# Optimization experiments

Measured on AMD Instinct MI355X. Metric: run time of the kernel, lower is better.

The kernel has to match this reference:

```python
import jax, jax.numpy as jnp
import numpy as np

MIN_NORM = 1e-15
BALL_EPS = 1e-5  # proj margin, c = 1
HYPER_BETA = 1.0


def _artanh(x):
    x = jnp.clip(x, -1.0 + 1e-7, 1.0 - 1e-7)
    return jnp.arctanh(x)


def _proj(x):
    # clip points inside the unit Poincare ball
    norm = jnp.maximum(jnp.linalg.norm(x, axis=-1, keepdims=True), MIN_NORM)
    maxnorm = 1.0 - BALL_EPS
    return jnp.where(norm > maxnorm, x / norm * maxnorm, x)


def _expmap0(u):
    un = jnp.maximum(jnp.linalg.norm(u, axis=-1, keepdims=True), MIN_NORM)
    return jnp.tanh(un) * u / un


def _mobius_add(x, y):
    x2 = jnp.sum(x * x, axis=-1, keepdims=True)
    y2 = jnp.sum(y * y, axis=-1, keepdims=True)
    xy = jnp.sum(x * y, axis=-1, keepdims=True)
    num = (1.0 + 2.0 * xy + y2) * x + (1.0 - x2) * y
    den = 1.0 + 2.0 * xy + x2 * y2
    return num / jnp.maximum(den, MIN_NORM)


def _sqdist(p, q):
    ma = _mobius_add(-p, q)
    d = 2.0 * _artanh(jnp.linalg.norm(ma, axis=-1))
    return d * d


def _to_klein(x):
    return 2.0 * x / (1.0 + jnp.sum(x * x, axis=-1, keepdims=True))


def _lorentz_factor(x):
    return 1.0 / jnp.sqrt(jnp.maximum(1.0 - jnp.sum(x * x, axis=-1), 1e-7))


def _klein_to(x):
    return x / (1.0 + jnp.sqrt(jnp.maximum(1.0 - jnp.sum(x * x, axis=-1, keepdims=True), 0.0)))


def _logmap0(p):
    pn = jnp.maximum(jnp.linalg.norm(p, axis=-1, keepdims=True), MIN_NORM)
    return _artanh(pn) * p / pn


def setup_inputs() -> dict:
    key = jax.random.key(0)
    k1, k2, k3, k4, k5 = jax.random.split(key, 5)
    B, L, V, D, A, S = 4096, 50, 50000, 200, 14, 30
    inputs = jax.random.randint(k1, (B, L), 0, V, dtype=jnp.int32)
    emb = jax.random.normal(k2, (V, D), dtype=jnp.float32) * 0.1  # w2v * 0.1 as in student_init
    xav = float(np.sqrt(6.0 / (D + D)))
    M = jax.random.uniform(k3, (D, D), dtype=jnp.float32, minval=-xav, maxval=xav)
    a_emb = jax.random.normal(k4, (A, S, D), dtype=jnp.float32) * 0.1
    sw = jax.random.uniform(k5, (A, S), dtype=jnp.float32)
    seed_w = sw / jnp.sum(jnp.abs(sw), axis=1, keepdims=True)  # L1-normalized
    return {"inputs": inputs, "emb": emb, "M": M, "a_emb": a_emb, "seed_w": seed_w}


def reference(inputs, emb, M, a_emb, seed_w):
    # --- AttentionEncoder ---
    x_wrd = emb[inputs]                                   # [B,L,D] gather
    x_avg = jnp.mean(x_wrd, axis=1)                       # [B,D]
    scores = jnp.einsum('bld,de,be->bl', x_wrd, M, x_avg)  # [B,L]
    a = jax.nn.softmax(scores, axis=1)
    enc = jnp.einsum('bl,bld->bd', a, x_wrd)              # [B,D]

    # --- hyperbolic projection ---
    enc = _proj(_expmap0(enc))                            # [B,D] on Poincare ball
    a_emb_w = jnp.sum(a_emb * seed_w[:, :, None], axis=1)  # [A,D]
    hyp_a = _proj(_expmap0(a_emb_w))                      # [A,D]

    sqd = _sqdist(enc[:, None, :], hyp_a[None, :, :])     # [B,A]
    probs_exp = jnp.exp(-HYPER_BETA * sqd - 0.05)         # [B,A]
    a_probs = probs_exp / jnp.sum(probs_exp, axis=1, keepdims=True)

    kle = _to_klein(hyp_a)                                # [A,D]
    lf = _lorentz_factor(kle)                             # [A]
    probs = lf[None, :] * probs_exp                       # [B,A]
    probs_expanded = (probs / jnp.sum(probs, axis=1, keepdims=True))[:, :, None]  # [B,A,1]

    kle_o = jnp.sum(kle[None, :, :] * probs_expanded, axis=1)  # [B,D] Klein barycenter
    r = _klein_to(kle_o)                                  # [B,D]
    eu_r = _logmap0(r)                                    # [B,D]
    return eu_r, probs_expanded, a_probs
```

## Files before the change

### kernel.cpp

```cpp
#include <hip/hip_runtime.h>
#include <hip/hip_fp16.h>
#include <math.h>

#define B_ 4096
#define L_ 50
#define D_ 200
#define A_ 14
#define S_ 30

#define WS_HYP   0
#define WS_KLE   (A_ * D_)
#define WS_Y2    (2 * A_ * D_)
#define WS_LF    (WS_Y2 + A_)
#define WS_MH    8192
#define WS_V     8192

__device__ __forceinline__ float wave_reduce_sum(float v) {
    #pragma unroll
    for (int off = 32; off > 0; off >>= 1) v += __shfl_down(v, off, 64);
    return v;
}
__device__ __forceinline__ float bfly_sum(float v) {
    #pragma unroll
    for (int m = 32; m > 0; m >>= 1) v += __shfl_xor(v, m, 64);
    return v;
}
__device__ __forceinline__ float bfly_max(float v) {
    #pragma unroll
    for (int m = 32; m > 0; m >>= 1) v = fmaxf(v, __shfl_xor(v, m, 64));
    return v;
}
__device__ __forceinline__ float bfly_sum16(float v) {
    #pragma unroll
    for (int m = 8; m > 0; m >>= 1) v += __shfl_xor(v, m, 64);
    return v;
}
__device__ __forceinline__ float block_reduce_512(float val, volatile float* red) {
    __syncthreads();
    val = wave_reduce_sum(val);
    if ((threadIdx.x & 63) == 0) red[threadIdx.x >> 6] = val;
    __syncthreads();
    float s = 0.f;
    #pragma unroll
    for (int i = 0; i < 8; ++i) s += red[i];
    return s;
}

typedef _Float16 h2v __attribute__((ext_vector_type(2)));
__device__ __forceinline__ float fd2(unsigned a, unsigned b, float c) {
#if __has_builtin(__builtin_amdgcn_fdot2)
    return __builtin_amdgcn_fdot2(__builtin_bit_cast(h2v, a),
                                  __builtin_bit_cast(h2v, b), c, false);
#else
    __half2 ha = __builtin_bit_cast(__half2, a), hb = __builtin_bit_cast(__half2, b);
    float2 fa = __half22float2(ha), fb = __half22float2(hb);
    return fmaf(fa.x, fb.x, fmaf(fa.y, fb.y, c));
#endif
}
__device__ __forceinline__ unsigned packh2(float a, float b) {
    __half2 h = __floats2half2_rn(a, b);
    return __builtin_bit_cast(unsigned, h);
}

__global__ __launch_bounds__(256) void precompute_anchors(
    const float* __restrict__ a_emb, const float* __restrict__ seed_w,
    float* __restrict__ ws)
{
    __shared__ float u[A_][D_];
    __shared__ float nrm2[A_];
    const int t = threadIdx.x;
    const int wave = t >> 6, lane = t & 63;

    for (int d = t; d < D_; d += 256) {
        for (int a = 0; a < A_; ++a) {
            float acc = 0.f;
            #pragma unroll 5
            for (int s = 0; s < S_; ++s)
                acc += a_emb[(a * S_ + s) * D_ + d] * seed_w[a * S_ + s];
            u[a][d] = acc;
        }
    }
    __syncthreads();

    for (int a = wave; a < A_; a += 4) {
        float s = 0.f;
        for (int d = lane; d < D_; d += 64) s += u[a][d] * u[a][d];
        s = wave_reduce_sum(s);
        if (lane == 0) nrm2[a] = s;
    }
    __syncthreads();

    float* hyp = ws + WS_HYP;
    float* kle = ws + WS_KLE;
    float* y2  = ws + WS_Y2;
    float* lf  = ws + WS_LF;
    const float maxn = 1.0f - 1e-5f;

    for (int a = 0; a < A_; ++a) {
        float un = fmaxf(sqrtf(nrm2[a]), 1e-15f);
        float th = tanhf(un);
        float pn = fminf(th, maxn);
        float s  = pn / un;
        float py2 = pn * pn;
        float kscale = 2.0f / (1.0f + py2);
        float k2 = py2 * kscale * kscale;
        if (t == 0) {
            y2[a] = py2;
            lf[a] = 1.0f / sqrtf(fmaxf(1.0f - k2, 1e-7f));
        }
        for (int d = t; d < D_; d += 256) {
            float h = u[a][d] * s;
            hyp[a * D_ + d] = h;
            kle[a * D_ + d] = h * kscale;
        }
    }
}

__global__ __launch_bounds__(256) void convert_M(
    const float* __restrict__ M, __half* __restrict__ Mh)
{
    int i = blockIdx.x * 256 + threadIdx.x;
    if (i < D_ * D_) Mh[i] = __float2half(M[i]);
}

__global__ __launch_bounds__(256) void fused_wave(
    const int*   __restrict__ inputs,
    const float* __restrict__ emb,
    const float* __restrict__ ws,
    float* __restrict__ out)
{
    const float*  kle = ws + WS_KLE;
    const float*  y2  = ws + WS_Y2;
    const float*  lf  = ws + WS_LF;
    const __half* Mh  = (const __half*)(ws + WS_MH);

    const int wid  = threadIdx.x >> 6, lane = threadIdx.x & 63;
    const int b    = blockIdx.x * 4 + wid;
    const bool L50 = (lane < 50);

    const int sidx = inputs[b * L_ + (L50 ? lane : 0)];

    float a0 = 0.f, a1 = 0.f, a2 = 0.f, a3 = 0.f;
    {
        const int off = L50 ? 4 * lane : 0;
        #pragma unroll 10
        for (int l = 0; l < L_; ++l) {
            const int row = __shfl(sidx, l, 64);
            float4 x = *(const float4*)(emb + (size_t)row * D_ + off);
            a0 += x.x; a1 += x.y; a2 += x.z; a3 += x.w;
        }
    }
    const float inv = 1.0f / (float)L_;
    unsigned xu0 = packh2(a0 * inv, a1 * inv);
    unsigned xu1 = packh2(a2 * inv, a3 * inv);

    float v0 = 0.f, v1 = 0.f, v2 = 0.f, v3 = 0.f;
    {
        const int mr = L50 ? 4 * lane : 0;
        const __half* m0 = Mh + (size_t)(mr + 0) * D_;
        const __half* m1 = Mh + (size_t)(mr + 1) * D_;
        const __half* m2 = Mh + (size_t)(mr + 2) * D_;
        const __half* m3 = Mh + (size_t)(mr + 3) * D_;
        #pragma unroll 5
        for (int c = 0; c < 25; ++c) {
            unsigned xa = __shfl(xu0, 2 * c,     64);
            unsigned xb = __shfl(xu1, 2 * c,     64);
            unsigned xc = __shfl(xu0, 2 * c + 1, 64);
            unsigned xd = __shfl(xu1, 2 * c + 1, 64);
            uint4 q0 = *(const uint4*)(m0 + 8 * c);
            uint4 q1 = *(const uint4*)(m1 + 8 * c);
            uint4 q2 = *(const uint4*)(m2 + 8 * c);
            uint4 q3 = *(const uint4*)(m3 + 8 * c);
            v0 = fd2(q0.x, xa, v0); v0 = fd2(q0.y, xb, v0); v0 = fd2(q0.z, xc, v0); v0 = fd2(q0.w, xd, v0);
            v1 = fd2(q1.x, xa, v1); v1 = fd2(q1.y, xb, v1); v1 = fd2(q1.z, xc, v1); v1 = fd2(q1.w, xd, v1);
            v2 = fd2(q2.x, xa, v2); v2 = fd2(q2.y, xb, v2); v2 = fd2(q2.z, xc, v2); v2 = fd2(q2.w, xd, v2);
            v3 = fd2(q3.x, xa, v3); v3 = fd2(q3.y, xb, v3); v3 = fd2(q3.z, xc, v3); v3 = fd2(q3.w, xd, v3);
        }
    }

    float s;
    {
        const float* xr = emb + (size_t)sidx * D_;
        float acc = 0.f;
        #pragma unroll 10
        for (int c = 0; c < 50; ++c) {
            float4 x = *(const float4*)(xr + 4 * c);
            float w0 = __shfl(v0, c, 64), w1 = __shfl(v1, c, 64);
            float w2 = __shfl(v2, c, 64), w3 = __shfl(v3, c, 64);
            acc = fmaf(x.x, w0, fmaf(x.y, w1, fmaf(x.z, w2, fmaf(x.w, w3, acc))));
        }
        s = L50 ? acc : -INFINITY;
    }

    const float mx = bfly_max(s);
    const float ex = L50 ? expf(s - mx) : 0.f;
    const float ssum = bfly_sum(ex);
    const float attnv = ex / ssum;

    float e0 = 0.f, e1 = 0.f, e2 = 0.f, e3 = 0.f;
    {
        const int off = L50 ? 4 * lane : 0;
        #pragma unroll 10
        for (int l = 0; l < L_; ++l) {
            const int row = __shfl(sidx, l, 64);
            const float w = __shfl(attnv, l, 64);
            float4 x = *(const float4*)(emb + (size_t)row * D_ + off);
            e0 = fmaf(w, x.x, e0); e1 = fmaf(w, x.y, e1);
            e2 = fmaf(w, x.z, e2); e3 = fmaf(w, x.w, e3);
        }
        if (!L50) { e0 = e1 = e2 = e3 = 0.f; }
    }

    const float n2 = bfly_sum(e0 * e0 + e1 * e1 + e2 * e2 + e3 * e3);
    const float un = fmaxf(sqrtf(n2), 1e-15f);
    const float pn = fminf(tanhf(un), 1.0f - 1e-5f);
    const float ps = pn / un;
    const float x2 = pn * pn;
    const float p0 = e0 * ps, p1 = e1 * ps, p2 = e2 * ps, p3 = e3 * ps;

    const int koff = L50 ? 4 * lane : 0;
    float kd = 0.f;
    #pragma unroll
    for (int a = 0; a < A_; ++a) {
        float4 k = *(const float4*)(kle + a * D_ + koff);
        float part = L50 ? (p0 * k.x + p1 * k.y + p2 * k.z + p3 * k.w) : 0.f;
        float d = bfly_sum(part);
        if (lane == a) kd = d;
    }

    float px = 0.f, lfv = 0.f;
    if (lane < A_) {
        const float yy  = y2[lane];
        lfv = lf[lane];
        const float dot = kd * (1.0f + yy) * 0.5f;
        const float c1 = 1.0f - 2.0f * dot + yy;
        const float c2 = 1.0f - x2;
        const float num2 = c1 * c1 * x2 - 2.0f * c1 * c2 * dot + c2 * c2 * yy;
        const float den  = fmaxf(1.0f - 2.0f * dot + x2 * yy, 1e-15f);
        const float nma  = sqrtf(fmaxf(num2, 0.f)) / den;
        const float z    = fminf(nma, 1.0f - 1e-7f);
        const float dist = logf((1.0f + z) / (1.0f - z));
        px = expf(-dist * dist - 0.05f);
    }
    const float se = bfly_sum16(px);
    const float sp = bfly_sum16(lfv * px);
    float pev = 0.f;
    if (lane < A_) {
        pev = lfv * px / sp;
        out[B_ * D_ + b * A_ + lane] = pev;
        out[B_ * D_ + B_ * A_ + b * A_ + lane] = px / se;
    }

    float k0 = 0.f, k1 = 0.f, k2 = 0.f, k3 = 0.f;
    #pragma unroll
    for (int a = 0; a < A_; ++a) {
        const float w = __shfl(pev, a, 64);
        float4 k = *(const float4*)(kle + a * D_ + koff);
        k0 = fmaf(w, k.x, k0); k1 = fmaf(w, k.y, k1);
        k2 = fmaf(w, k.z, k2); k3 = fmaf(w, k.w, k3);
    }
    if (!L50) { k0 = k1 = k2 = k3 = 0.f; }
    const float n2k = bfly_sum(k0 * k0 + k1 * k1 + k2 * k2 + k3 * k3);
    const float denom = 1.0f + sqrtf(fmaxf(1.0f - n2k, 0.f));
    const float r2 = n2k / (denom * denom);
    const float rn = fmaxf(sqrtf(r2), 1e-15f);
    const float z2 = fminf(rn, 1.0f - 1e-7f);
    const float fac = 0.5f * logf((1.0f + z2) / (1.0f - z2)) / rn;
    if (L50) {
        float4 o = make_float4(fac * k0 / denom, fac * k1 / denom,
                               fac * k2 / denom, fac * k3 / denom);
        *(float4*)(out + (size_t)b * D_ + 4 * lane) = o;
    }
}

#define G_R 8
__global__ __launch_bounds__(512) void gather_gemm(
    const int* __restrict__ inputs, const float* __restrict__ emb,
    const float* __restrict__ M, float* __restrict__ ws)
{
    __shared__ __align__(16) float xs[G_R][D_ + 4];
    __shared__ int sidx[G_R][L_];
    float* v = ws + WS_V;
    const int b0 = blockIdx.x * G_R;
    const int t = threadIdx.x;
    const int wave = t >> 6, lane = t & 63;

    for (int p = t; p < G_R * L_; p += 512) sidx[p / L_][p % L_] = inputs[b0 * L_ + p];
    __syncthreads();

    if (lane < D_ / 4) {
        float ax = 0.f, ay = 0.f, az = 0.f, aw = 0.f;
        #pragma unroll
        for (int l = 0; l < L_; ++l) {
            const float4 vv = ((const float4*)(emb + (size_t)sidx[wave][l] * D_))[lane];
            ax += vv.x; ay += vv.y; az += vv.z; aw += vv.w;
        }
        const float inv = 1.0f / (float)L_;
        ((float4*)xs[wave])[lane] = make_float4(ax * inv, ay * inv, az * inv, aw * inv);
    }
    __syncthreads();

    const int r = t & 7, dg = t >> 3;
    const float4* xr4 = (const float4*)xs[r];
    #pragma unroll
    for (int k = 0; k < 4; ++k) {
        const int d = dg + 64 * k;
        if (d < D_) {
            const float4* Mr4 = (const float4*)(M + d * D_);
            float acc = 0.f;
            #pragma unroll
            for (int e = 0; e < D_ / 4; ++e) {
                float4 m4 = Mr4[e], x4 = xr4[e];
                acc += m4.x * x4.x + m4.y * x4.y + m4.z * x4.z + m4.w * x4.w;
            }
            v[(size_t)(b0 + r) * D_ + d] = acc;
        }
    }
}

__global__ __launch_bounds__(512, 8) void fused_main(
    const int*   __restrict__ inputs,
    const float* __restrict__ emb,
    const float* __restrict__ ws,
    float* __restrict__ out)
{
    __shared__ __align__(16) float x[L_][D_];
    __shared__ float attn[L_];
    __shared__ int   sidx[L_];
    __shared__ float red[8];
    __shared__ float sums[2];

    const float* hyp = ws + WS_HYP;
    const float* kle = ws + WS_KLE;
    const float* y2  = ws + WS_Y2;
    const float* lf  = ws + WS_LF;
    const float* vg  = ws + WS_V;

    const int b = blockIdx.x;
    const int t = threadIdx.x;
    const int wave = t >> 6, lane = t & 63;

    float vr0 = vg[(size_t)b * D_ + lane];
    float vr1 = vg[(size_t)b * D_ + lane + 64];
    float vr2 = vg[(size_t)b * D_ + lane + 128];
    float vr3 = (lane < D_ - 192) ? vg[(size_t)b * D_ + lane + 192] : 0.f;

    if (t < L_) sidx[t] = inputs[b * L_ + t];
    __syncthreads();

    {
        const int DQ = D_ / 4;
        const int p0 = t, p1 = t + 512, p2 = t + 1024, p3 = t + 1536, p4 = t + 2048;
        const bool has4 = (p4 < L_ * DQ);
        float4 a0 = ((const float4*)(emb + (size_t)sidx[p0 / DQ] * D_))[p0 % DQ];
        float4 a1 = ((const float4*)(emb + (size_t)sidx[p1 / DQ] * D_))[p1 % DQ];
        float4 a2 = ((const float4*)(emb + (size_t)sidx[p2 / DQ] * D_))[p2 % DQ];
        float4 a3 = ((const float4*)(emb + (size_t)sidx[p3 / DQ] * D_))[p3 % DQ];
        float4 a4;
        if (has4) a4 = ((const float4*)(emb + (size_t)sidx[p4 / DQ] * D_))[p4 % DQ];
        ((float4*)x[p0 / DQ])[p0 % DQ] = a0;
        ((float4*)x[p1 / DQ])[p1 % DQ] = a1;
        ((float4*)x[p2 / DQ])[p2 % DQ] = a2;
        ((float4*)x[p3 / DQ])[p3 % DQ] = a3;
        if (has4) ((float4*)x[p4 / DQ])[p4 % DQ] = a4;
    }
    __syncthreads();

    for (int l = wave; l < L_; l += 8) {
        float s = x[l][lane] * vr0 + x[l][lane + 64] * vr1 + x[l][lane + 128] * vr2;
        if (lane < D_ - 192) s += x[l][lane + 192] * vr3;
        s = wave_reduce_sum(s);
        if (lane == 0) attn[l] = s;
    }
    __syncthreads();

    if (wave == 0) {
        float scv = (lane < L_) ? attn[lane] : -INFINITY;
        float m = scv;
        #pragma unroll
        for (int off = 32; off > 0; off >>= 1) m = fmaxf(m, __shfl_xor(m, off, 64));
        float e = (lane < L_) ? expf(scv - m) : 0.f;
        float ss = e;
        #pragma unroll
        for (int off = 32; off > 0; off >>= 1) ss += __shfl_xor(ss, off, 64);
        if (lane < L_) attn[lane] = e / ss;
    }
    __syncthreads();

    float encv = 0.f;
    if (t < D_) {
        #pragma unroll 10
        for (int l = 0; l < L_; ++l) encv += attn[l] * x[l][t];
    }

    float n2 = block_reduce_512((t < D_) ? encv * encv : 0.f, red);
    const float maxn = 1.0f - 1e-5f;
    float un = fmaxf(sqrtf(n2), 1e-15f);
    float pn = fminf(tanhf(un), maxn);
    float ps = pn / un;
    float x2 = pn * pn;
    float* pvec  = &x[0][0];
    float* dotpq = &x[1][0];
    float* pexp  = &x[1][16];
    float* pe    = &x[1][32];
    if (t < D_) pvec[t] = encv * ps;
    __syncthreads();

    for (int a = wave; a < A_; a += 8) {
        const float* ha = hyp + a * D_;
        float s = ha[lane] * pvec[lane] + ha[lane + 64] * pvec[lane + 64]
                + ha[lane + 128] * pvec[lane + 128];
        if (lane < D_ - 192) s += ha[lane + 192] * pvec[lane + 192];
        s = wave_reduce_sum(s);
        if (lane == 0) dotpq[a] = s;
    }
    __syncthreads();

    if (t < A_) {
        float dot = dotpq[t];
        float yy  = y2[t];
        float c1 = 1.0f - 2.0f * dot + yy;
        float c2 = 1.0f - x2;
        float num2 = c1 * c1 * x2 - 2.0f * c1 * c2 * dot + c2 * c2 * yy;
        float den  = fmaxf(1.0f - 2.0f * dot + x2 * yy, 1e-15f);
        float nma  = sqrtf(fmaxf(num2, 0.f)) / den;
        float z    = fminf(nma, 1.0f - 1e-7f);
        float dist = logf((1.0f + z) / (1.0f - z));
        pexp[t] = expf(-dist * dist - 0.05f);
    }
    __syncthreads();
    if (t == 0) {
        float se = 0.f, sp = 0.f;
        for (int a = 0; a < A_; ++a) { se += pexp[a]; sp += lf[a] * pexp[a]; }
        sums[0] = 1.0f / se;
        sums[1] = 1.0f / sp;
    }
    __syncthreads();
    if (t < A_) {
        float ap  = pexp[t] * sums[0];
        float pev = lf[t] * pexp[t] * sums[1];
        pe[t] = pev;
        out[B_ * D_ + b * A_ + t] = pev;
        out[B_ * D_ + B_ * A_ + b * A_ + t] = ap;
    }
    __syncthreads();

    float ko = 0.f;
    if (t < D_) {
        #pragma unroll
        for (int a = 0; a < A_; ++a) ko += kle[a * D_ + t] * pe[a];
    }
    float n2k = block_reduce_512((t < D_) ? ko * ko : 0.f, red);
    if (t < D_) {
        float denom = 1.0f + sqrtf(fmaxf(1.0f - n2k, 0.f));
        float rv = ko / denom;
        float r2 = n2k / (denom * denom);
        float rn = fmaxf(sqrtf(r2), 1e-15f);
        float z  = fminf(rn, 1.0f - 1e-7f);
        float fac = (0.5f * logf((1.0f + z) / (1.0f - z))) / rn;
        out[b * D_ + t] = fac * rv;
    }
}

extern "C" void kernel_launch(void* const* d_in, const int* in_sizes, int n_in,
                              void* d_out, int out_size, void* d_ws, size_t ws_size,
                              hipStream_t stream) {
    (void)in_sizes; (void)n_in; (void)out_size;
    const int*   inputs = (const int*)  d_in[0];
    const float* emb    = (const float*)d_in[1];
    const float* M      = (const float*)d_in[2];
    const float* a_emb  = (const float*)d_in[3];
    const float* seed_w = (const float*)d_in[4];
    float* out = (float*)d_out;
    float* ws  = (float*)d_ws;

    precompute_anchors<<<1, 256, 0, stream>>>(a_emb, seed_w, ws);

    const size_t need = (size_t)(WS_MH + (D_ * D_ + 1) / 2) * sizeof(float);
    if (ws_size >= need) {
        __half* Mh = (__half*)(ws + WS_MH);
        convert_M<<<(D_ * D_ + 255) / 256, 256, 0, stream>>>(M, Mh);
        fused_wave<<<B_ / 4, 256, 0, stream>>>(inputs, emb, ws, out);
    } else {
        gather_gemm<<<B_ / G_R, 512, 0, stream>>>(inputs, emb, M, ws);
        fused_main<<<B_, 512, 0, stream>>>(inputs, emb, ws, out);
    }
}
```

Measured before the change: 127.2 us.

## Fuse score computation into weighted-sum pass with online softmax

Removes the separate per-lane full-row scoring pass, which read whole embedding rows per lane, and the separate softmax. Each word's score is now a butterfly-reduced dot of the same float4 slice already loaded for the weighted sum, with an online-softmax rescale, and the next row is prefetched. This saves one full pass over the gathered rows, at the cost of 50 serial cross-lane reductions and per-step expf calls on the critical path.

```diff
diff --git a/kernel.cpp b/kernel.cpp
--- a/kernel.cpp
+++ b/kernel.cpp
@@ -23,11 +23,6 @@
 __device__ __forceinline__ float bfly_sum(float v) {
     #pragma unroll
     for (int m = 32; m > 0; m >>= 1) v += __shfl_xor(v, m, 64);
-    return v;
-}
-__device__ __forceinline__ float bfly_max(float v) {
-    #pragma unroll
-    for (int m = 32; m > 0; m >>= 1) v = fmaxf(v, __shfl_xor(v, m, 64));
     return v;
 }
 __device__ __forceinline__ float bfly_sum16(float v) {
@@ -139,10 +134,10 @@
     const bool L50 = (lane < 50);
 
     const int sidx = inputs[b * L_ + (L50 ? lane : 0)];
+    const int off  = L50 ? 4 * lane : 0;
 
     float a0 = 0.f, a1 = 0.f, a2 = 0.f, a3 = 0.f;
     {
-        const int off = L50 ? 4 * lane : 0;
         #pragma unroll 10
         for (int l = 0; l < L_; ++l) {
             const int row = __shfl(sidx, l, 64);
@@ -178,36 +173,33 @@
         }
     }
 
-    float s;
-    {
-        const float* xr = emb + (size_t)sidx * D_;
-        float acc = 0.f;
-        #pragma unroll 10
-        for (int c = 0; c < 50; ++c) {
-            float4 x = *(const float4*)(xr + 4 * c);
-            float w0 = __shfl(v0, c, 64), w1 = __shfl(v1, c, 64);
-            float w2 = __shfl(v2, c, 64), w3 = __shfl(v3, c, 64);
-            acc = fmaf(x.x, w0, fmaf(x.y, w1, fmaf(x.z, w2, fmaf(x.w, w3, acc))));
-        }
-        s = L50 ? acc : -INFINITY;
-    }
-
-    const float mx = bfly_max(s);
-    const float ex = L50 ? expf(s - mx) : 0.f;
-    const float ssum = bfly_sum(ex);
-    const float attnv = ex / ssum;
-
+    float m = -INFINITY, ssum = 0.f;
     float e0 = 0.f, e1 = 0.f, e2 = 0.f, e3 = 0.f;
     {
-        const int off = L50 ? 4 * lane : 0;
+        const int r0 = __shfl(sidx, 0, 64);
+        float4 x = *(const float4*)(emb + (size_t)r0 * D_ + off);
         #pragma unroll 10
         for (int l = 0; l < L_; ++l) {
-            const int row = __shfl(sidx, l, 64);
-            const float w = __shfl(attnv, l, 64);
-            float4 x = *(const float4*)(emb + (size_t)row * D_ + off);
+            float4 xn;
+            if (l + 1 < L_) {
+                const int rn = __shfl(sidx, l + 1, 64);
+                xn = *(const float4*)(emb + (size_t)rn * D_ + off);
+            }
+            float part = L50 ? (x.x * v0 + x.y * v1 + x.z * v2 + x.w * v3) : 0.f;
+            const float s = bfly_sum(part);
+            if (s > m) {
+                const float r = expf(m - s);
+                ssum *= r; e0 *= r; e1 *= r; e2 *= r; e3 *= r;
+                m = s;
+            }
+            const float w = expf(s - m);
+            ssum += w;
             e0 = fmaf(w, x.x, e0); e1 = fmaf(w, x.y, e1);
             e2 = fmaf(w, x.z, e2); e3 = fmaf(w, x.w, e3);
-        }
+            x = xn;
+        }
+        const float rs = 1.0f / ssum;
+        e0 *= rs; e1 *= rs; e2 *= rs; e3 *= rs;
         if (!L50) { e0 = e1 = e2 = e3 = 0.f; }
     }
 
@@ -218,7 +210,7 @@
     const float x2 = pn * pn;
     const float p0 = e0 * ps, p1 = e1 * ps, p2 = e2 * ps, p3 = e3 * ps;
 
-    const int koff = L50 ? 4 * lane : 0;
+    const int koff = off;
     float kd = 0.f;
     #pragma unroll
     for (int a = 0; a < A_; ++a) {
```

After: 122.1 us. -4.0%, faster.

## Process one batch row per block and stage gathered embeddings in shared memory

Applied to the files above, without the earlier changes.

Switches from one wavefront per batch row to a 256-thread block per row. The gathered embedding rows are cached in LDS as fp16, so the score and weighted-sum passes no longer re-gather from global memory, which previously happened three times. The L loop is split across four waves with partial sums reduced through shared memory, and the M·x_avg GEMV is split across two waves. In exchange it adds block barriers, extra LDS traffic and fp16 rounding of the embeddings used for scores and the attention sum. It also runs the anchor stage redundantly in every wave, with only wave 0 writing outputs.

```diff
diff --git a/kernel.cpp b/kernel.cpp
--- a/kernel.cpp
+++ b/kernel.cpp
@@ -123,44 +123,71 @@
     if (i < D_ * D_) Mh[i] = __float2half(M[i]);
 }
 
-__global__ __launch_bounds__(256) void fused_wave(
+__global__ __launch_bounds__(256, 6) void fused_block(
     const int*   __restrict__ inputs,
     const float* __restrict__ emb,
     const float* __restrict__ ws,
     float* __restrict__ out)
 {
+    __shared__ __align__(8) __half xh[L_][D_];
+    __shared__ float part[4][D_];
+    __shared__ float vsh[D_];
+    __shared__ float scores[64];
+
     const float*  kle = ws + WS_KLE;
     const float*  y2  = ws + WS_Y2;
     const float*  lf  = ws + WS_LF;
     const __half* Mh  = (const __half*)(ws + WS_MH);
 
     const int wid  = threadIdx.x >> 6, lane = threadIdx.x & 63;
-    const int b    = blockIdx.x * 4 + wid;
+    const int b    = blockIdx.x;
     const bool L50 = (lane < 50);
 
     const int sidx = inputs[b * L_ + (L50 ? lane : 0)];
-
-    float a0 = 0.f, a1 = 0.f, a2 = 0.f, a3 = 0.f;
+    const int off  = L50 ? 4 * lane : 0;
+
     {
-        const int off = L50 ? 4 * lane : 0;
-        #pragma unroll 10
-        for (int l = 0; l < L_; ++l) {
-            const int row = __shfl(sidx, l, 64);
-            float4 x = *(const float4*)(emb + (size_t)row * D_ + off);
-            a0 += x.x; a1 += x.y; a2 += x.z; a3 += x.w;
-        }
-    }
-    const float inv = 1.0f / (float)L_;
-    unsigned xu0 = packh2(a0 * inv, a1 * inv);
-    unsigned xu1 = packh2(a2 * inv, a3 * inv);
-
-    float v0 = 0.f, v1 = 0.f, v2 = 0.f, v3 = 0.f;
-    {
-        const int mr = L50 ? 4 * lane : 0;
+        float a0 = 0.f, a1 = 0.f, a2 = 0.f, a3 = 0.f;
+        #pragma unroll
+        for (int j = 0; j < 13; ++j) {
+            const int l = wid + 4 * j;
+            if (l < L_) {
+                const int row = __shfl(sidx, l, 64);
+                float4 x = *(const float4*)(emb + (size_t)row * D_ + off);
+                a0 += x.x; a1 += x.y; a2 += x.z; a3 += x.w;
+                if (L50) {
+                    uint2 u;
+                    u.x = packh2(x.x, x.y);
+                    u.y = packh2(x.z, x.w);
+                    *(uint2*)&xh[l][4 * lane] = u;
+                }
+            }
+        }
+        if (L50) {
+            part[wid][4 * lane + 0] = a0;
+            part[wid][4 * lane + 1] = a1;
+            part[wid][4 * lane + 2] = a2;
+            part[wid][4 * lane + 3] = a3;
+        }
+    }
+    __syncthreads();
+
+    unsigned xu0 = 0, xu1 = 0;
+    if (L50) {
+        const float inv = 1.0f / (float)L_;
+        float f0 = (part[0][4*lane+0] + part[1][4*lane+0] + part[2][4*lane+0] + part[3][4*lane+0]) * inv;
+        float f1 = (part[0][4*lane+1] + part[1][4*lane+1] + part[2][4*lane+1] + part[3][4*lane+1]) * inv;
+        float f2 = (part[0][4*lane+2] + part[1][4*lane+2] + part[2][4*lane+2] + part[3][4*lane+2]) * inv;
+        float f3 = (part[0][4*lane+3] + part[1][4*lane+3] + part[2][4*lane+3] + part[3][4*lane+3]) * inv;
+        xu0 = packh2(f0, f1);
+        xu1 = packh2(f2, f3);
+    }
+
+    if (wid < 2) {
+        float w0 = 0.f, w1 = 0.f;
+        const int mr = 100 * wid + 2 * (L50 ? lane : 0);
         const __half* m0 = Mh + (size_t)(mr + 0) * D_;
         const __half* m1 = Mh + (size_t)(mr + 1) * D_;
-        const __half* m2 = Mh + (size_t)(mr + 2) * D_;
-        const __half* m3 = Mh + (size_t)(mr + 3) * D_;
         #pragma unroll 5
         for (int c = 0; c < 25; ++c) {
             unsigned xa = __shfl(xu0, 2 * c,     64);
@@ -169,46 +196,74 @@
             unsigned xd = __shfl(xu1, 2 * c + 1, 64);
             uint4 q0 = *(const uint4*)(m0 + 8 * c);
             uint4 q1 = *(const uint4*)(m1 + 8 * c);
-            uint4 q2 = *(const uint4*)(m2 + 8 * c);
-            uint4 q3 = *(const uint4*)(m3 + 8 * c);
-            v0 = fd2(q0.x, xa, v0); v0 = fd2(q0.y, xb, v0); v0 = fd2(q0.z, xc, v0); v0 = fd2(q0.w, xd, v0);
-            v1 = fd2(q1.x, xa, v1); v1 = fd2(q1.y, xb, v1); v1 = fd2(q1.z, xc, v1); v1 = fd2(q1.w, xd, v1);
-            v2 = fd2(q2.x, xa, v2); v2 = fd2(q2.y, xb, v2); v2 = fd2(q2.z, xc, v2); v2 = fd2(q2.w, xd, v2);
-            v3 = fd2(q3.x, xa, v3); v3 = fd2(q3.y, xb, v3); v3 = fd2(q3.z, xc, v3); v3 = fd2(q3.w, xd, v3);
-        }
-    }
-
-    float s;
-    {
-        const float* xr = emb + (size_t)sidx * D_;
-        float acc = 0.f;
-        #pragma unroll 10
-        for (int c = 0; c < 50; ++c) {
-            float4 x = *(const float4*)(xr + 4 * c);
-            float w0 = __shfl(v0, c, 64), w1 = __shfl(v1, c, 64);
-            float w2 = __shfl(v2, c, 64), w3 = __shfl(v3, c, 64);
-            acc = fmaf(x.x, w0, fmaf(x.y, w1, fmaf(x.z, w2, fmaf(x.w, w3, acc))));
-        }
-        s = L50 ? acc : -INFINITY;
-    }
-
-    const float mx = bfly_max(s);
-    const float ex = L50 ? expf(s - mx) : 0.f;
-    const float ssum = bfly_sum(ex);
-    const float attnv = ex / ssum;
+            w0 = fd2(q0.x, xa, w0); w0 = fd2(q0.y, xb, w0); w0 = fd2(q0.z, xc, w0); w0 = fd2(q0.w, xd, w0);
+            w1 = fd2(q1.x, xa, w1); w1 = fd2(q1.y, xb, w1); w1 = fd2(q1.z, xc, w1); w1 = fd2(q1.w, xd, w1);
+        }
+        if (L50) { vsh[mr] = w0; vsh[mr + 1] = w1; }
+    }
+    __syncthreads();
+
+    float v0 = 0.f, v1 = 0.f, v2 = 0.f, v3 = 0.f;
+    if (L50) {
+        v0 = vsh[4 * lane + 0];
+        v1 = vsh[4 * lane + 1];
+        v2 = vsh[4 * lane + 2];
+        v3 = vsh[4 * lane + 3];
+    }
+
+    #pragma unroll
+    for (int j = 0; j < 13; ++j) {
+        const int l = wid + 4 * j;
+        if (l < L_) {
+            float p = 0.f;
+            if (L50) {
+                uint2 u = *(const uint2*)&xh[l][4 * lane];
+                float2 f0 = __half22float2(__builtin_bit_cast(__half2, u.x));
+                float2 f1 = __half22float2(__builtin_bit_cast(__half2, u.y));
+                p = f0.x * v0 + f0.y * v1 + f1.x * v2 + f1.y * v3;
+            }
+            const float s = bfly_sum(p);
+            if (lane == 0) scores[l] = s;
+        }
+    }
+    __syncthreads();
+
+    const float sv = L50 ? scores[lane] : -INFINITY;
+    const float mx = bfly_max(sv);
+    const float ex = L50 ? expf(sv - mx) : 0.f;
+    const float sm = bfly_sum(ex);
+    const float attnv = ex / sm;
 
     float e0 = 0.f, e1 = 0.f, e2 = 0.f, e3 = 0.f;
-    {
-        const int off = L50 ? 4 * lane : 0;
-        #pragma unroll 10
-        for (int l = 0; l < L_; ++l) {
-            const int row = __shfl(sidx, l, 64);
-            const float w = __shfl(attnv, l, 64);
-            float4 x = *(const float4*)(emb + (size_t)row * D_ + off);
-            e0 = fmaf(w, x.x, e0); e1 = fmaf(w, x.y, e1);
-            e2 = fmaf(w, x.z, e2); e3 = fmaf(w, x.w, e3);
-        }
-        if (!L50) { e0 = e1 = e2 = e3 = 0.f; }
+    #pragma unroll
+    for (int j = 0; j < 13; ++j) {
+        const int l = wid + 4 * j;
+        if (l < L_) {
+            const float wl = __shfl(attnv, l, 64);
+            if (L50) {
+                uint2 u = *(const uint2*)&xh[l][4 * lane];
+                float2 f0 = __half22float2(__builtin_bit_cast(__half2, u.x));
+                float2 f1 = __half22float2(__builtin_bit_cast(__half2, u.y));
+                e0 = fmaf(wl, f0.x, e0); e1 = fmaf(wl, f0.y, e1);
+                e2 = fmaf(wl, f1.x, e2); e3 = fmaf(wl, f1.y, e3);
+            }
+        }
+    }
+    __syncthreads();
+    if (L50) {
+        part[wid][4 * lane + 0] = e0;
+        part[wid][4 * lane + 1] = e1;
+        part[wid][4 * lane + 2] = e2;
+        part[wid][4 * lane + 3] = e3;
+    }
+    __syncthreads();
+    if (L50) {
+        e0 = part[0][4*lane+0] + part[1][4*lane+0] + part[2][4*lane+0] + part[3][4*lane+0];
+        e1 = part[0][4*lane+1] + part[1][4*lane+1] + part[2][4*lane+1] + part[3][4*lane+1];
+        e2 = part[0][4*lane+2] + part[1][4*lane+2] + part[2][4*lane+2] + part[3][4*lane+2];
+        e3 = part[0][4*lane+3] + part[1][4*lane+3] + part[2][4*lane+3] + part[3][4*lane+3];
+    } else {
+        e0 = e1 = e2 = e3 = 0.f;
     }
 
     const float n2 = bfly_sum(e0 * e0 + e1 * e1 + e2 * e2 + e3 * e3);
@@ -218,13 +273,12 @@
     const float x2 = pn * pn;
     const float p0 = e0 * ps, p1 = e1 * ps, p2 = e2 * ps, p3 = e3 * ps;
 
-    const int koff = L50 ? 4 * lane : 0;
     float kd = 0.f;
     #pragma unroll
     for (int a = 0; a < A_; ++a) {
-        float4 k = *(const float4*)(kle + a * D_ + koff);
-        float part = L50 ? (p0 * k.x + p1 * k.y + p2 * k.z + p3 * k.w) : 0.f;
-        float d = bfly_sum(part);
+        float4 k = *(const float4*)(kle + a * D_ + off);
+        float p = L50 ? (p0 * k.x + p1 * k.y + p2 * k.z + p3 * k.w) : 0.f;
+        float d = bfly_sum(p);
         if (lane == a) kd = d;
     }
 
@@ -247,15 +301,17 @@
     float pev = 0.f;
     if (lane < A_) {
         pev = lfv * px / sp;
-        out[B_ * D_ + b * A_ + lane] = pev;
-        out[B_ * D_ + B_ * A_ + b * A_ + lane] = px / se;
+        if (wid == 0) {
+            out[B_ * D_ + b * A_ + lane] = pev;
+            out[B_ * D_ + B_ * A_ + b * A_ + lane] = px / se;
+        }
     }
 
     float k0 = 0.f, k1 = 0.f, k2 = 0.f, k3 = 0.f;
     #pragma unroll
     for (int a = 0; a < A_; ++a) {
         const float w = __shfl(pev, a, 64);
-        float4 k = *(const float4*)(kle + a * D_ + koff);
+        float4 k = *(const float4*)(kle + a * D_ + off);
         k0 = fmaf(w, k.x, k0); k1 = fmaf(w, k.y, k1);
         k2 = fmaf(w, k.z, k2); k3 = fmaf(w, k.w, k3);
     }
@@ -266,7 +322,7 @@
     const float rn = fmaxf(sqrtf(r2), 1e-15f);
     const float z2 = fminf(rn, 1.0f - 1e-7f);
     const float fac = 0.5f * logf((1.0f + z2) / (1.0f - z2)) / rn;
-    if (L50) {
+    if (L50 && wid == 0) {
         float4 o = make_float4(fac * k0 / denom, fac * k1 / denom,
                                fac * k2 / denom, fac * k3 / denom);
         *(float4*)(out + (size_t)b * D_ + 4 * lane) = o;
@@ -480,7 +536,7 @@
     if (ws_size >= need) {
         __half* Mh = (__half*)(ws + WS_MH);
         convert_M<<<(D_ * D_ + 255) / 256, 256, 0, stream>>>(M, Mh);
-        fused_wave<<<B_ / 4, 256, 0, stream>>>(inputs, emb, ws, out);
+        fused_block<<<B_, 256, 0, stream>>>(inputs, emb, ws, out);
     } else {
         gather_gemm<<<B_ / G_R, 512, 0, stream>>>(inputs, emb, M, ws);
         fused_main<<<B_, 512, 0, stream>>>(inputs, emb, ws, out);
```

Result: slower. 145.0 us (+14.0%).
